# Performance work log

Measured on AMD Instinct MI355X. Metric: run time of the kernel, lower is better.

## Reference

```python
import jax, jax.numpy as jnp
import numpy as np

H = 128          # hidden_channels
N_USER = 100000
N_ITEM = 50000
E = 1000000      # number of labeled edges


def setup_inputs() -> dict:
    key = jax.random.key(0)
    ks = jax.random.split(key, 6)
    z_user = jax.random.normal(ks[0], (N_USER, H), dtype=jnp.float32)
    z_item = jax.random.normal(ks[1], (N_ITEM, H), dtype=jnp.float32)
    row = jax.random.randint(ks[2], (E,), 0, N_USER, dtype=jnp.int64 if jax.config.jax_enable_x64 else jnp.int32)
    col = jax.random.randint(ks[3], (E,), 0, N_ITEM, dtype=jnp.int64 if jax.config.jax_enable_x64 else jnp.int32)
    W1 = jax.random.normal(ks[4], (2 * H, H), dtype=jnp.float32) / np.sqrt(2 * H)
    b1 = jnp.zeros((H,), dtype=jnp.float32)
    W2 = jax.random.normal(ks[5], (H, 1), dtype=jnp.float32) / np.sqrt(H)
    b2 = jnp.zeros((1,), dtype=jnp.float32)
    return {"z_user": z_user, "z_item": z_item, "row": row, "col": col,
            "W1": W1, "b1": b1, "W2": W2, "b2": b2}


def reference(z_user, z_item, row, col, W1, b1, W2, b2):
    # z = cat([z_user[row], z_item[col]], -1); lin1(z).relu(); lin2 -> view(-1)
    # Split W1 so we never materialize the [E, 2H] concat explicitly as one buffer:
    # cat([a, b]) @ W1 == a @ W1[:H] + b @ W1[H:]
    W1u, W1i = W1[:H], W1[H:]
    h = z_user[row] @ W1u + z_item[col] @ W1i + b1          # [E, H]
    h = jax.nn.relu(h)
    out = h @ W2 + b2                                        # [E, 1]
    return out.reshape(-1)
```

## Files before the change

kernel.cpp:

```cpp
#include <hip/hip_runtime.h>

#define HH 128

typedef __attribute__((ext_vector_type(8))) short bf16x8;
typedef __attribute__((ext_vector_type(4))) float f32x4;

__device__ inline unsigned short f2bf(float f) {
    unsigned u = __builtin_bit_cast(unsigned, f);
    u += 0x7FFF + ((u >> 16) & 1);
    return (unsigned short)(u >> 16);
}

__global__ __launch_bounds__(256) void project_both_kernel(
    const float* __restrict__ Zu, const float* __restrict__ Zi,
    const float* __restrict__ W1, const float* __restrict__ b1,
    unsigned short* __restrict__ Pu, unsigned short* __restrict__ Pi,
    int n_user, int n_item, int ublocks)
{
    __shared__ unsigned short sWt[128 * 128];
    __shared__ unsigned short sOut[64 * 136];

    const bool isUser = ((int)blockIdx.x < ublocks);
    const float* __restrict__ Z = isUser ? Zu : Zi;
    const float* __restrict__ W = isUser ? W1 : (W1 + HH * HH);
    unsigned short* __restrict__ P = isUser ? Pu : Pi;
    const int nrows  = isUser ? n_user : n_item;
    const int ntiles = (nrows + 63) >> 6;
    const int tbase  = (isUser ? (int)blockIdx.x : ((int)blockIdx.x - ublocks)) * 2;

    const int t    = threadIdx.x;
    const int wave = t >> 6;
    const int lane = t & 63;
    const int l16  = lane & 15;
    const int lk8  = (lane >> 4) * 8;

    #pragma unroll 4
    for (int i = 0; i < 16; ++i) {
        int idx = t + i * 256;
        int k   = idx >> 5;
        int c4  = (idx & 31) * 4;
        float4 w = *(const float4*)(W + (size_t)k * HH + c4);
        float wv[4] = {w.x, w.y, w.z, w.w};
        #pragma unroll
        for (int j = 0; j < 4; ++j) {
            int c = c4 + j;
            sWt[c * 128 + (((k >> 3) ^ (c & 15)) << 3) + (k & 7)] = f2bf(wv[j]);
        }
    }

    float b1r[8];
    #pragma unroll
    for (int nt = 0; nt < 8; ++nt)
        b1r[nt] = isUser ? b1[nt * 16 + l16] : 0.f;

    __syncthreads();

    #pragma unroll 1
    for (int s = 0; s < 2; ++s) {
        const int tile = tbase + s;
        if (tile >= ntiles) break;
        const int rbase = tile << 6;

        f32x4 acc[8];
        #pragma unroll
        for (int nt = 0; nt < 8; ++nt) acc[nt] = (f32x4)0.f;

        int m = rbase + wave * 16 + l16;
        if (m > nrows - 1) m = nrows - 1;
        const float* Zrow = Z + (size_t)m * HH;

        #pragma unroll
        for (int kk = 0; kk < 4; ++kk) {
            float4 z0 = *(const float4*)(Zrow + kk * 32 + lk8);
            float4 z1 = *(const float4*)(Zrow + kk * 32 + lk8 + 4);
            bf16x8 a;
            a[0] = (short)f2bf(z0.x); a[1] = (short)f2bf(z0.y);
            a[2] = (short)f2bf(z0.z); a[3] = (short)f2bf(z0.w);
            a[4] = (short)f2bf(z1.x); a[5] = (short)f2bf(z1.y);
            a[6] = (short)f2bf(z1.z); a[7] = (short)f2bf(z1.w);

            const int chunkSw = ((kk * 4 + (lane >> 4)) ^ l16) << 3;
            #pragma unroll
            for (int nt = 0; nt < 8; ++nt) {
                int c = nt * 16 + l16;
                bf16x8 b = *(const bf16x8*)(sWt + c * 128 + chunkSw);
                acc[nt] = __builtin_amdgcn_mfma_f32_16x16x32_bf16(a, b, acc[nt], 0, 0, 0);
            }
        }

        __syncthreads();
        #pragma unroll
        for (int nt = 0; nt < 8; ++nt) {
            int colc = nt * 16 + l16;
            #pragma unroll
            for (int r = 0; r < 4; ++r) {
                int orow = wave * 16 + (lane >> 4) * 4 + r;
                sOut[orow * 136 + colc] = f2bf(acc[nt][r] + b1r[nt]);
            }
        }
        __syncthreads();
        #pragma unroll
        for (int i = 0; i < 4; ++i) {
            int idx = t + i * 256;
            int r   = idx >> 4;
            int ch  = idx & 15;
            int grow = rbase + r;
            if (grow < nrows)
                *(uint4*)(P + (size_t)grow * HH + ch * 8) =
                    *(const uint4*)(sOut + r * 136 + ch * 8);
        }
    }
}

__global__ __launch_bounds__(256) void edge_bf16_kernel(
    const unsigned short* __restrict__ Pu, const unsigned short* __restrict__ Pi,
    const int* __restrict__ row, const int* __restrict__ col,
    const float* __restrict__ W2, const float* __restrict__ b2,
    float* __restrict__ out, int E)
{
    const int lane16 = threadIdx.x & 15;
    const int gid    = (blockIdx.x * blockDim.x + threadIdx.x) >> 4;
    const int stride = (gridDim.x * blockDim.x) >> 4;
    const int c0     = lane16 * 8;

    float w2r[8];
    #pragma unroll
    for (int j = 0; j < 8; ++j) w2r[j] = W2[c0 + j];
    const float b2s = b2[0];

    int e = gid;
    for (; e + stride < E; e += 2 * stride) {
        const int e2 = e + stride;
        int u0 = row[e],  i0 = col[e];
        int u1 = row[e2], i1 = col[e2];
        uint4 pu0 = *(const uint4*)(Pu + (size_t)u0 * HH + c0);
        uint4 pi0 = *(const uint4*)(Pi + (size_t)i0 * HH + c0);
        uint4 pu1 = *(const uint4*)(Pu + (size_t)u1 * HH + c0);
        uint4 pi1 = *(const uint4*)(Pi + (size_t)i1 * HH + c0);

        unsigned a0[4] = {pu0.x, pu0.y, pu0.z, pu0.w};
        unsigned b0[4] = {pi0.x, pi0.y, pi0.z, pi0.w};
        unsigned a1[4] = {pu1.x, pu1.y, pu1.z, pu1.w};
        unsigned b1w[4] = {pi1.x, pi1.y, pi1.z, pi1.w};

        float p0 = 0.f, p1 = 0.f;
        #pragma unroll
        for (int q = 0; q < 4; ++q) {
            float x0 = __builtin_bit_cast(float, a0[q] << 16);
            float x1 = __builtin_bit_cast(float, a0[q] & 0xFFFF0000u);
            float y0 = __builtin_bit_cast(float, b0[q] << 16);
            float y1 = __builtin_bit_cast(float, b0[q] & 0xFFFF0000u);
            p0 = fmaf(fmaxf(x0 + y0, 0.f), w2r[2 * q],     p0);
            p0 = fmaf(fmaxf(x1 + y1, 0.f), w2r[2 * q + 1], p0);
            float u0f = __builtin_bit_cast(float, a1[q] << 16);
            float u1f = __builtin_bit_cast(float, a1[q] & 0xFFFF0000u);
            float v0f = __builtin_bit_cast(float, b1w[q] << 16);
            float v1f = __builtin_bit_cast(float, b1w[q] & 0xFFFF0000u);
            p1 = fmaf(fmaxf(u0f + v0f, 0.f), w2r[2 * q],     p1);
            p1 = fmaf(fmaxf(u1f + v1f, 0.f), w2r[2 * q + 1], p1);
        }
        #pragma unroll
        for (int m = 8; m >= 1; m >>= 1) {
            p0 += __shfl_xor(p0, m, 64);
            p1 += __shfl_xor(p1, m, 64);
        }
        if (lane16 == 0) { out[e] = p0 + b2s; out[e2] = p1 + b2s; }
    }
    if (e < E) {
        int u = row[e], it = col[e];
        uint4 pu = *(const uint4*)(Pu + (size_t)u  * HH + c0);
        uint4 pi = *(const uint4*)(Pi + (size_t)it * HH + c0);
        unsigned a[4] = {pu.x, pu.y, pu.z, pu.w};
        unsigned b[4] = {pi.x, pi.y, pi.z, pi.w};
        float p = 0.f;
        #pragma unroll
        for (int q = 0; q < 4; ++q) {
            float x0 = __builtin_bit_cast(float, a[q] << 16);
            float x1 = __builtin_bit_cast(float, a[q] & 0xFFFF0000u);
            float y0 = __builtin_bit_cast(float, b[q] << 16);
            float y1 = __builtin_bit_cast(float, b[q] & 0xFFFF0000u);
            p = fmaf(fmaxf(x0 + y0, 0.f), w2r[2 * q],     p);
            p = fmaf(fmaxf(x1 + y1, 0.f), w2r[2 * q + 1], p);
        }
        #pragma unroll
        for (int m = 8; m >= 1; m >>= 1)
            p += __shfl_xor(p, m, 64);
        if (lane16 == 0) out[e] = p + b2s;
    }
}

__global__ __launch_bounds__(256) void edge_direct_kernel(
    const float* __restrict__ zu, const float* __restrict__ zi,
    const int* __restrict__ row, const int* __restrict__ col,
    const float* __restrict__ W1, const float* __restrict__ b1,
    const float* __restrict__ W2, const float* __restrict__ b2,
    float* __restrict__ out, int E)
{
    const int lane   = threadIdx.x & 31;
    const int gid    = (blockIdx.x * blockDim.x + threadIdx.x) >> 5;
    const int stride = (gridDim.x * blockDim.x) >> 5;
    const int c0     = lane * 4;

    const float4 b1v = *(const float4*)(b1 + c0);
    const float4 w2v = *(const float4*)(W2 + c0);
    const float  b2s = b2[0];

    for (int e = gid; e < E; e += stride) {
        int u  = row[e];
        int it = col[e];
        const float* zur = zu + (size_t)u  * HH;
        const float* zir = zi + (size_t)it * HH;
        float4 acc = b1v;
        for (int k = 0; k < HH; ++k) {
            float  zk = zur[k];
            float4 w  = *(const float4*)(W1 + (size_t)k * HH + c0);
            acc.x = fmaf(zk, w.x, acc.x);
            acc.y = fmaf(zk, w.y, acc.y);
            acc.z = fmaf(zk, w.z, acc.z);
            acc.w = fmaf(zk, w.w, acc.w);
        }
        for (int k = 0; k < HH; ++k) {
            float  zk = zir[k];
            float4 w  = *(const float4*)(W1 + (size_t)(HH + k) * HH + c0);
            acc.x = fmaf(zk, w.x, acc.x);
            acc.y = fmaf(zk, w.y, acc.y);
            acc.z = fmaf(zk, w.z, acc.z);
            acc.w = fmaf(zk, w.w, acc.w);
        }
        float p = fmaxf(acc.x, 0.f) * w2v.x;
        p = fmaf(fmaxf(acc.y, 0.f), w2v.y, p);
        p = fmaf(fmaxf(acc.z, 0.f), w2v.z, p);
        p = fmaf(fmaxf(acc.w, 0.f), w2v.w, p);
        #pragma unroll
        for (int m = 16; m >= 1; m >>= 1)
            p += __shfl_xor(p, m, 64);
        if (lane == 0) out[e] = p + b2s;
    }
}

extern "C" void kernel_launch(void* const* d_in, const int* in_sizes, int n_in,
                              void* d_out, int out_size, void* d_ws, size_t ws_size,
                              hipStream_t stream)
{
    const float* z_user = (const float*)d_in[0];
    const float* z_item = (const float*)d_in[1];
    const int*   row    = (const int*)d_in[2];
    const int*   col    = (const int*)d_in[3];
    const float* W1     = (const float*)d_in[4];
    const float* b1     = (const float*)d_in[5];
    const float* W2     = (const float*)d_in[6];
    const float* b2     = (const float*)d_in[7];
    float*       out    = (float*)d_out;

    const int n_user = in_sizes[0] / HH;
    const int n_item = in_sizes[1] / HH;
    const int E      = in_sizes[2];

    const size_t need = ((size_t)n_user + (size_t)n_item) * HH * sizeof(unsigned short);
    if (ws_size >= need) {
        unsigned short* Pu = (unsigned short*)d_ws;
        unsigned short* Pi = Pu + (size_t)n_user * HH;
        const int utiles  = (n_user + 63) >> 6;
        const int itiles  = (n_item + 63) >> 6;
        const int ublocks = (utiles + 1) >> 1;
        const int iblocks = (itiles + 1) >> 1;
        project_both_kernel<<<ublocks + iblocks, 256, 0, stream>>>(
            z_user, z_item, W1, b1, Pu, Pi, n_user, n_item, ublocks);
        edge_bf16_kernel<<<2048, 256, 0, stream>>>(Pu, Pi, row, col, W2, b2, out, E);
    } else {
        edge_direct_kernel<<<2048, 256, 0, stream>>>(z_user, z_item, row, col, W1, b1, W2, b2, out, E);
    }
}
```

Measured before the change: 106.1 us.

## Counting-sort edges by user row before bf16 gather edge kernel

Adds a per-call counting sort of edges by user index (atomic histogram, three-stage scan, atomic scatter into packed 64-bit keys). The edge kernel then walks contiguous sorted ranges so consecutive edges reuse the same user projection row. It also simplifies the fallback edge loop by removing the 2x manual unroll. The intent is better cache locality on the user gathers, at the cost of several extra launches, atomics, an 8-byte-per-edge sorted buffer, and scattered output writes.

```diff
diff --git a/kernel.cpp b/kernel.cpp
--- a/kernel.cpp
+++ b/kernel.cpp
@@ -4,6 +4,7 @@
 
 typedef __attribute__((ext_vector_type(8))) short bf16x8;
 typedef __attribute__((ext_vector_type(4))) float f32x4;
+typedef unsigned long long u64;
 
 __device__ inline unsigned short f2bf(float f) {
     unsigned u = __builtin_bit_cast(unsigned, f);
@@ -112,6 +113,126 @@
     }
 }
 
+__global__ __launch_bounds__(256) void hist_kernel(
+    const int* __restrict__ row, unsigned* __restrict__ hist, int E)
+{
+    int i  = blockIdx.x * blockDim.x + threadIdx.x;
+    int st = gridDim.x * blockDim.x;
+    for (int e = i; e < E; e += st) atomicAdd(&hist[row[e]], 1u);
+}
+
+__global__ __launch_bounds__(256) void scan1_kernel(
+    const unsigned* __restrict__ hist, unsigned* __restrict__ cursor,
+    unsigned* __restrict__ bsums, int n)
+{
+    __shared__ unsigned s[256];
+    const int t = threadIdx.x;
+    const int start = blockIdx.x * 2048 + t * 8;
+    unsigned v[8]; unsigned tsum = 0;
+    #pragma unroll
+    for (int j = 0; j < 8; ++j) {
+        int idx = start + j;
+        v[j] = (idx < n) ? hist[idx] : 0u;
+        tsum += v[j];
+    }
+    s[t] = tsum; __syncthreads();
+    for (int off = 1; off < 256; off <<= 1) {
+        unsigned x = (t >= off) ? s[t - off] : 0u;
+        __syncthreads();
+        s[t] += x;
+        __syncthreads();
+    }
+    if (t == 255) bsums[blockIdx.x] = s[255];
+    unsigned run = s[t] - tsum;
+    #pragma unroll
+    for (int j = 0; j < 8; ++j) {
+        int idx = start + j;
+        if (idx < n) cursor[idx] = run;
+        run += v[j];
+    }
+}
+
+__global__ __launch_bounds__(256) void scan2_kernel(unsigned* __restrict__ bsums, int nb)
+{
+    __shared__ unsigned s[256];
+    const int t = threadIdx.x;
+    unsigned v = (t < nb) ? bsums[t] : 0u;
+    s[t] = v; __syncthreads();
+    for (int off = 1; off < 256; off <<= 1) {
+        unsigned x = (t >= off) ? s[t - off] : 0u;
+        __syncthreads();
+        s[t] += x;
+        __syncthreads();
+    }
+    if (t < nb) bsums[t] = s[t] - v;
+}
+
+__global__ __launch_bounds__(256) void scan3_kernel(
+    unsigned* __restrict__ cursor, const unsigned* __restrict__ bsums, int n)
+{
+    int i  = blockIdx.x * blockDim.x + threadIdx.x;
+    int st = gridDim.x * blockDim.x;
+    for (int k = i; k < n; k += st) cursor[k] += bsums[k >> 11];
+}
+
+__global__ __launch_bounds__(256) void scatter_kernel(
+    const int* __restrict__ row, const int* __restrict__ col,
+    unsigned* __restrict__ cursor, u64* __restrict__ srt, int E)
+{
+    int i  = blockIdx.x * blockDim.x + threadIdx.x;
+    int st = gridDim.x * blockDim.x;
+    for (int e = i; e < E; e += st) {
+        int u = row[e];
+        unsigned pos = atomicAdd(&cursor[u], 1u);
+        srt[pos] = ((u64)(unsigned)u << 37) | ((u64)(unsigned)col[e] << 20) | (u64)(unsigned)e;
+    }
+}
+
+__global__ __launch_bounds__(256) void edge_sorted_kernel(
+    const unsigned short* __restrict__ Pu, const unsigned short* __restrict__ Pi,
+    const u64* __restrict__ srt, const float* __restrict__ W2,
+    const float* __restrict__ b2, float* __restrict__ out, int E)
+{
+    const int lane16 = threadIdx.x & 15;
+    const int c0     = lane16 * 8;
+    const int g      = (blockIdx.x * blockDim.x + threadIdx.x) >> 4;
+    const int ng     = (gridDim.x * blockDim.x) >> 4;
+    const int per    = (E + ng - 1) / ng;
+    int s = g * per;
+    int t = s + per; if (t > E) t = E;
+
+    float w2r[8];
+    #pragma unroll
+    for (int j = 0; j < 8; ++j) w2r[j] = W2[c0 + j];
+    const float b2s = b2[0];
+
+    #pragma unroll 2
+    for (int e = s; e < t; ++e) {
+        u64 pk = srt[e];
+        int u   = (int)(pk >> 37);
+        int ic  = (int)((pk >> 20) & 0x1FFFF);
+        int eid = (int)(pk & 0xFFFFF);
+        uint4 pu = *(const uint4*)(Pu + (size_t)u  * HH + c0);
+        uint4 pi = *(const uint4*)(Pi + (size_t)ic * HH + c0);
+        unsigned a[4] = {pu.x, pu.y, pu.z, pu.w};
+        unsigned b[4] = {pi.x, pi.y, pi.z, pi.w};
+        float p = 0.f;
+        #pragma unroll
+        for (int q = 0; q < 4; ++q) {
+            float x0 = __builtin_bit_cast(float, a[q] << 16);
+            float x1 = __builtin_bit_cast(float, a[q] & 0xFFFF0000u);
+            float y0 = __builtin_bit_cast(float, b[q] << 16);
+            float y1 = __builtin_bit_cast(float, b[q] & 0xFFFF0000u);
+            p = fmaf(fmaxf(x0 + y0, 0.f), w2r[2 * q],     p);
+            p = fmaf(fmaxf(x1 + y1, 0.f), w2r[2 * q + 1], p);
+        }
+        #pragma unroll
+        for (int m = 8; m >= 1; m >>= 1)
+            p += __shfl_xor(p, m, 64);
+        if (lane16 == 0) out[eid] = p + b2s;
+    }
+}
+
 __global__ __launch_bounds__(256) void edge_bf16_kernel(
     const unsigned short* __restrict__ Pu, const unsigned short* __restrict__ Pi,
     const int* __restrict__ row, const int* __restrict__ col,
@@ -128,45 +249,7 @@
     for (int j = 0; j < 8; ++j) w2r[j] = W2[c0 + j];
     const float b2s = b2[0];
 
-    int e = gid;
-    for (; e + stride < E; e += 2 * stride) {
-        const int e2 = e + stride;
-        int u0 = row[e],  i0 = col[e];
-        int u1 = row[e2], i1 = col[e2];
-        uint4 pu0 = *(const uint4*)(Pu + (size_t)u0 * HH + c0);
-        uint4 pi0 = *(const uint4*)(Pi + (size_t)i0 * HH + c0);
-        uint4 pu1 = *(const uint4*)(Pu + (size_t)u1 * HH + c0);
-        uint4 pi1 = *(const uint4*)(Pi + (size_t)i1 * HH + c0);
-
-        unsigned a0[4] = {pu0.x, pu0.y, pu0.z, pu0.w};
-        unsigned b0[4] = {pi0.x, pi0.y, pi0.z, pi0.w};
-        unsigned a1[4] = {pu1.x, pu1.y, pu1.z, pu1.w};
-        unsigned b1w[4] = {pi1.x, pi1.y, pi1.z, pi1.w};
-
-        float p0 = 0.f, p1 = 0.f;
-        #pragma unroll
-        for (int q = 0; q < 4; ++q) {
-            float x0 = __builtin_bit_cast(float, a0[q] << 16);
-            float x1 = __builtin_bit_cast(float, a0[q] & 0xFFFF0000u);
-            float y0 = __builtin_bit_cast(float, b0[q] << 16);
-            float y1 = __builtin_bit_cast(float, b0[q] & 0xFFFF0000u);
-            p0 = fmaf(fmaxf(x0 + y0, 0.f), w2r[2 * q],     p0);
-            p0 = fmaf(fmaxf(x1 + y1, 0.f), w2r[2 * q + 1], p0);
-            float u0f = __builtin_bit_cast(float, a1[q] << 16);
-            float u1f = __builtin_bit_cast(float, a1[q] & 0xFFFF0000u);
-            float v0f = __builtin_bit_cast(float, b1w[q] << 16);
-            float v1f = __builtin_bit_cast(float, b1w[q] & 0xFFFF0000u);
-            p1 = fmaf(fmaxf(u0f + v0f, 0.f), w2r[2 * q],     p1);
-            p1 = fmaf(fmaxf(u1f + v1f, 0.f), w2r[2 * q + 1], p1);
-        }
-        #pragma unroll
-        for (int m = 8; m >= 1; m >>= 1) {
-            p0 += __shfl_xor(p0, m, 64);
-            p1 += __shfl_xor(p1, m, 64);
-        }
-        if (lane16 == 0) { out[e] = p0 + b2s; out[e2] = p1 + b2s; }
-    }
-    if (e < E) {
+    for (int e = gid; e < E; e += stride) {
         int u = row[e], it = col[e];
         uint4 pu = *(const uint4*)(Pu + (size_t)u  * HH + c0);
         uint4 pi = *(const uint4*)(Pi + (size_t)it * HH + c0);
@@ -238,6 +321,8 @@
     }
 }
 
+static inline size_t align256(size_t x) { return (x + 255) & ~(size_t)255; }
+
 extern "C" void kernel_launch(void* const* d_in, const int* in_sizes, int n_in,
                               void* d_out, int out_size, void* d_ws, size_t ws_size,
                               hipStream_t stream)
@@ -256,10 +341,45 @@
     const int n_item = in_sizes[1] / HH;
     const int E      = in_sizes[2];
 
-    const size_t need = ((size_t)n_user + (size_t)n_item) * HH * sizeof(unsigned short);
-    if (ws_size >= need) {
-        unsigned short* Pu = (unsigned short*)d_ws;
-        unsigned short* Pi = Pu + (size_t)n_user * HH;
+    const size_t offPu   = 0;
+    const size_t offPi   = align256(offPu + (size_t)n_user * HH * 2);
+    const size_t offSrt  = align256(offPi + (size_t)n_item * HH * 2);
+    const size_t offCur  = align256(offSrt + (size_t)E * 8);
+    const size_t offBs   = align256(offCur + (size_t)n_user * 4);
+    const size_t offHist = align256(offBs + 1024 * 4);
+    const size_t needSort = align256(offHist + (size_t)n_user * 4);
+    const size_t needProj = align256(offPi + (size_t)n_item * HH * 2);
+
+    const int nb1 = (n_user + 2047) >> 11;
+    const bool sortable = (E <= (1 << 20)) && (n_user <= (1 << 17)) &&
+                          (n_item <= (1 << 17)) && (nb1 <= 256) &&
+                          (ws_size >= needSort);
+
+    if (sortable) {
+        unsigned short* Pu   = (unsigned short*)((char*)d_ws + offPu);
+        unsigned short* Pi   = (unsigned short*)((char*)d_ws + offPi);
+        u64*            srt  = (u64*)((char*)d_ws + offSrt);
+        unsigned*       cur  = (unsigned*)((char*)d_ws + offCur);
+        unsigned*       bs   = (unsigned*)((char*)d_ws + offBs);
+        unsigned*       hist = (unsigned*)((char*)d_ws + offHist);
+
+        hipMemsetAsync(hist, 0, (size_t)n_user * 4, stream);
+        hist_kernel<<<1024, 256, 0, stream>>>(row, hist, E);
+        scan1_kernel<<<nb1, 256, 0, stream>>>(hist, cur, bs, n_user);
+        scan2_kernel<<<1, 256, 0, stream>>>(bs, nb1);
+        scan3_kernel<<<256, 256, 0, stream>>>(cur, bs, n_user);
+        scatter_kernel<<<1024, 256, 0, stream>>>(row, col, cur, srt, E);
+
+        const int utiles  = (n_user + 63) >> 6;
+        const int itiles  = (n_item + 63) >> 6;
+        const int ublocks = (utiles + 1) >> 1;
+        const int iblocks = (itiles + 1) >> 1;
+        project_both_kernel<<<ublocks + iblocks, 256, 0, stream>>>(
+            z_user, z_item, W1, b1, Pu, Pi, n_user, n_item, ublocks);
+        edge_sorted_kernel<<<2048, 256, 0, stream>>>(Pu, Pi, srt, W2, b2, out, E);
+    } else if (ws_size >= needProj) {
+        unsigned short* Pu = (unsigned short*)((char*)d_ws + offPu);
+        unsigned short* Pi = (unsigned short*)((char*)d_ws + offPi);
         const int utiles  = (n_user + 63) >> 6;
         const int itiles  = (n_item + 63) >> 6;
         const int ublocks = (utiles + 1) >> 1;
```

Measured after the change: 227.7 us. 2.15x slower.
